# Kernel tuning notes

Hardware: AMD Instinct MI355X
Metric: run time of the kernel (lower is better)

## Reference

```python
import jax, jax.numpy as jnp
import numpy as np

C, C_H, N_HEAD = 256, 32, 8
LN_EPS = 1e-5


def setup_inputs() -> dict:
    key = jax.random.key(0)
    ks = jax.random.split(key, 10)
    B, S, I = 1, 256, 384
    hc = C_H * N_HEAD
    w = lambda k, shp: (jax.random.normal(k, shp, dtype=jnp.float32) * 0.02)
    return {
        "m": jax.random.normal(ks[0], (B, S, I, C), dtype=jnp.float32),
        "msa_mask": jnp.ones((B, S, I), dtype=jnp.float32),
        "gamma": jnp.ones((C,), dtype=jnp.float32),
        "beta": jnp.zeros((C,), dtype=jnp.float32),
        "Wq": w(ks[1], (C, hc)),
        "Wk": w(ks[2], (C, hc)),
        "Wv": w(ks[3], (C, hc)),
        "Wg": w(ks[4], (C, hc)),
        "bg": jnp.zeros((hc,), dtype=jnp.float32),
        "Wo": w(ks[5], (hc, C)),
        "bo": jnp.zeros((C,), dtype=jnp.float32),
    }


def reference(m, msa_mask, gamma, beta, Wq, Wk, Wv, Wg, bg, Wo, bo):
    B, S, I, _ = m.shape
    h, ch = N_HEAD, C_H
    # LayerNorm over channel dim
    mu = jnp.mean(m, axis=-1, keepdims=True)
    var = jnp.mean((m - mu) ** 2, axis=-1, keepdims=True)
    x = (m - mu) * jax.lax.rsqrt(var + LN_EPS) * gamma + beta  # (B,s,i,c)
    # projections -> (B,s,i,h,ch)
    q = (x @ Wq).reshape(B, S, I, h, ch)
    k = (x @ Wk).reshape(B, S, I, h, ch)
    v = (x @ Wv).reshape(B, S, I, h, ch)
    gate = jax.nn.sigmoid(x @ Wg + bg).reshape(B, S, I, h, ch)
    # column-wise attention over s, per column i and head h
    a = jnp.einsum("bsihc,btihc->bihst", q, k) / np.float32(np.sqrt(ch))
    # additive mask bias: msa_mask (B,s,i) -> (B,i,s) -> (B,i,1,1,s)
    bias = (1e9 * (jnp.swapaxes(msa_mask, -1, -2) - 1.0))[:, :, None, None, :]
    a = jax.nn.softmax(a + bias, axis=-1)
    # weighted values -> (B,s,i,h,ch)
    o = jnp.einsum("bihst,btihc->bsihc", a, v)
    o = (gate * o).reshape(B, S, I, h * ch)
    return o @ Wo + bo
```

## Files before the change

### kernel.cpp

```cpp
#include <hip/hip_runtime.h>

typedef unsigned short ushort_t;
typedef __attribute__((ext_vector_type(4))) short short4v;
typedef __attribute__((ext_vector_type(8))) short short8;
typedef __attribute__((ext_vector_type(4))) float floatx4;

#define SEQ 256
#define NI 384
#define CDIM 256
#define NH 8
#define CH 32
#define HC 256
#define NROW (SEQ * NI)
#define QKVG_N 1024

__device__ __forceinline__ float b2f(ushort_t u) {
  union { unsigned int i; float f; } z;
  z.i = ((unsigned int)u) << 16;
  return z.f;
}
__device__ __forceinline__ ushort_t f2b(float f) {
  union { float f; unsigned int i; } z;
  z.f = f;
  unsigned int x = z.i;
  unsigned int r = (x + 0x7fffu + ((x >> 16) & 1u)) >> 16;
  return (ushort_t)r;
}
__device__ __forceinline__ float ldx(const void* p, size_t i, int f32) {
  if (f32) return ((const float*)p)[i];
  return b2f(((const ushort_t*)p)[i]);
}

__global__ void detect_kernel(const unsigned int* __restrict__ g, int* __restrict__ flag) {
  *flag = (g[0] == 0x3F800000u) ? 1 : 0;
}

__global__ __launch_bounds__(256) void ln_norm_kernel(
    const void* __restrict__ m, const void* __restrict__ gamma, const void* __restrict__ beta,
    const int* __restrict__ pflag, ushort_t* __restrict__ xln) {
  int f32 = *pflag;
  int wave = threadIdx.x >> 6, lane = threadIdx.x & 63;
  int row = blockIdx.x * 4 + wave;
  size_t base = (size_t)row * CDIM + lane * 4;
  float v[4];
  float s1 = 0.f, s2 = 0.f;
  #pragma unroll
  for (int j = 0; j < 4; ++j) {
    v[j] = ldx(m, base + j, f32);
    s1 += v[j]; s2 += v[j] * v[j];
  }
  #pragma unroll
  for (int off = 1; off < 64; off <<= 1) {
    s1 += __shfl_xor(s1, off);
    s2 += __shfl_xor(s2, off);
  }
  float mu = s1 * (1.0f / CDIM);
  float var = s2 * (1.0f / CDIM) - mu * mu;
  float rstd = rsqrtf(var + 1e-5f);
  short4v o;
  #pragma unroll
  for (int j = 0; j < 4; ++j) {
    float g = ldx(gamma, lane * 4 + j, f32);
    float b = ldx(beta, lane * 4 + j, f32);
    o[j] = (short)f2b((v[j] - mu) * rstd * g + b);
  }
  *(short4v*)(xln + base) = o;
}

__global__ void transpose5(const void* a0, const void* a1, const void* a2, const void* a3,
                           const void* a4, const int* __restrict__ pflag,
                           ushort_t* __restrict__ Wqkvg, ushort_t* __restrict__ WoT) {
  int f32 = *pflag;
  int z = blockIdx.z;
  const void* src = (z == 0) ? a0 : (z == 1) ? a1 : (z == 2) ? a2 : (z == 3) ? a3 : a4;
  int x = blockIdx.x * 16 + threadIdx.x;
  int y = blockIdx.y * 16 + threadIdx.y;
  ushort_t val = f2b(ldx(src, (size_t)y * 256 + x, f32));
  if (z < 4) Wqkvg[((size_t)z * 256 + x) * 256 + y] = val;
  else       WoT[(size_t)x * 256 + y] = val;
}

#define LDT 56

__global__ __launch_bounds__(256) void gemm128(
    const ushort_t* __restrict__ A, const ushort_t* __restrict__ Bt,
    void* __restrict__ C, const void* __restrict__ bias, const int* __restrict__ pflag,
    int N, int epi, int CW, int i0, int mapA, int mapC) {
  int flag = *pflag;
  __shared__ __align__(16) ushort_t lA[128 * LDT];
  __shared__ __align__(16) ushort_t lB[128 * LDT];
  int tid = threadIdx.x;
  int m0 = blockIdx.x * 128, n0 = blockIdx.y * 128;
  int wave = tid >> 6, lane = tid & 63, lr = lane & 15, lq = lane >> 4;
  int wr = wave >> 1, wc = wave & 1;

  floatx4 acc[4][4];
  #pragma unroll
  for (int a = 0; a < 4; ++a)
    #pragma unroll
    for (int b = 0; b < 4; ++b) {
      acc[a][b][0] = 0.f; acc[a][b][1] = 0.f; acc[a][b][2] = 0.f; acc[a][b][3] = 0.f;
    }

  int row = tid >> 1, koff = (tid & 1) * 16;
  int rloc = m0 + row;
  int growA = mapA ? ((rloc / CW) * NI + i0 + (rloc % CW)) : rloc;
  const ushort_t* Ap = A + (size_t)growA * CDIM + koff;
  const ushort_t* Bp = Bt + (size_t)(n0 + row) * CDIM + koff;

  for (int k0 = 0; k0 < CDIM; k0 += 32) {
    short8 a0 = *(const short8*)(Ap + k0);
    short8 a1 = *(const short8*)(Ap + k0 + 8);
    short8 b0 = *(const short8*)(Bp + k0);
    short8 b1 = *(const short8*)(Bp + k0 + 8);
    *(short8*)&lA[row * LDT + koff] = a0;
    *(short8*)&lA[row * LDT + koff + 8] = a1;
    *(short8*)&lB[row * LDT + koff] = b0;
    *(short8*)&lB[row * LDT + koff + 8] = b1;
    __syncthreads();
    short8 af[4], bf[4];
    #pragma unroll
    for (int jm = 0; jm < 4; ++jm)
      af[jm] = *(const short8*)&lA[(wr * 64 + jm * 16 + lr) * LDT + lq * 8];
    #pragma unroll
    for (int jn = 0; jn < 4; ++jn)
      bf[jn] = *(const short8*)&lB[(wc * 64 + jn * 16 + lr) * LDT + lq * 8];
    #pragma unroll
    for (int jm = 0; jm < 4; ++jm)
      #pragma unroll
      for (int jn = 0; jn < 4; ++jn)
        acc[jm][jn] = __builtin_amdgcn_mfma_f32_16x16x32_bf16(af[jm], bf[jn], acc[jm][jn], 0, 0, 0);
    __syncthreads();
  }

  #pragma unroll
  for (int jm = 0; jm < 4; ++jm) {
    #pragma unroll
    for (int jn = 0; jn < 4; ++jn) {
      int col = n0 + wc * 64 + jn * 16 + lr;
      #pragma unroll
      for (int r = 0; r < 4; ++r) {
        int rl = m0 + wr * 64 + jm * 16 + lq * 4 + r;
        float val = acc[jm][jn][r];
        if (epi == 1) {
          if (col >= 768) {
            val += ldx(bias, col - 768, flag);
            val = 1.0f / (1.0f + __expf(-val));
          }
          ((ushort_t*)C)[(size_t)rl * N + col] = f2b(val);
        } else {
          val += ldx(bias, col, flag);
          int g = mapC ? ((rl / CW) * NI + i0 + (rl % CW)) : rl;
          if (flag) ((float*)C)[(size_t)g * N + col] = val;
          else      ((ushort_t*)C)[(size_t)g * N + col] = f2b(val);
        }
      }
    }
  }
}

#define KSTR 56
#define VSTR 264
#define PSTR 264

__global__ __launch_bounds__(256) void attn_mfma(
    const ushort_t* __restrict__ qkvg, const void* __restrict__ mask,
    const int* __restrict__ pflag, ushort_t* __restrict__ xln, int CW, int i0) {
  int f32 = *pflag;
  int il = blockIdx.x, h = blockIdx.y, qt = blockIdx.z;
  __shared__ __align__(16) ushort_t Kl[SEQ * KSTR];
  __shared__ __align__(16) ushort_t Vt[CH * VSTR];
  __shared__ __align__(16) ushort_t Pl[4 * 16 * PSTR];
  __shared__ float biasS[SEQ];
  int tid = threadIdx.x;

  {
    int t = tid;
    size_t base = ((size_t)t * CW + il) * QKVG_N + h * CH;
    short8 kv[4], vv[4];
    #pragma unroll
    for (int c4 = 0; c4 < 4; ++c4) {
      kv[c4] = *(const short8*)(qkvg + base + 256 + c4 * 8);
      vv[c4] = *(const short8*)(qkvg + base + 512 + c4 * 8);
    }
    #pragma unroll
    for (int c4 = 0; c4 < 4; ++c4) *(short8*)&Kl[t * KSTR + c4 * 8] = kv[c4];
    #pragma unroll
    for (int c4 = 0; c4 < 4; ++c4)
      #pragma unroll
      for (int j = 0; j < 8; ++j)
        Vt[(c4 * 8 + j) * VSTR + t] = (ushort_t)vv[c4][j];
    biasS[t] = 1e9f * (ldx(mask, (size_t)t * NI + i0 + il, f32) - 1.0f);
  }
  __syncthreads();

  int wave = tid >> 6, lane = tid & 63, lr = lane & 15, quad = lane >> 4;
  int sbase = qt * 64 + wave * 16;
  short8 qf = *(const short8*)(qkvg + ((size_t)(sbase + lr) * CW + il) * QKVG_N + h * CH + quad * 8);

  const float scale = 0.17677669529663687f;
  floatx4 s[16];
  #pragma unroll
  for (int tt = 0; tt < 16; ++tt) {
    short8 kb = *(const short8*)&Kl[(tt * 16 + lr) * KSTR + quad * 8];
    floatx4 z;
    z[0] = 0.f; z[1] = 0.f; z[2] = 0.f; z[3] = 0.f;
    s[tt] = __builtin_amdgcn_mfma_f32_16x16x32_bf16(qf, kb, z, 0, 0, 0);
  }
  #pragma unroll
  for (int tt = 0; tt < 16; ++tt) {
    float bv = biasS[tt * 16 + lr];
    #pragma unroll
    for (int r = 0; r < 4; ++r) s[tt][r] = s[tt][r] * scale + bv;
  }

  float mr[4], ls[4];
  #pragma unroll
  for (int r = 0; r < 4; ++r) {
    mr[r] = s[0][r];
    #pragma unroll
    for (int tt = 1; tt < 16; ++tt) mr[r] = fmaxf(mr[r], s[tt][r]);
  }
  #pragma unroll
  for (int msk = 1; msk < 16; msk <<= 1)
    #pragma unroll
    for (int r = 0; r < 4; ++r) mr[r] = fmaxf(mr[r], __shfl_xor(mr[r], msk));
  #pragma unroll
  for (int tt = 0; tt < 16; ++tt)
    #pragma unroll
    for (int r = 0; r < 4; ++r) s[tt][r] = __expf(s[tt][r] - mr[r]);
  #pragma unroll
  for (int r = 0; r < 4; ++r) {
    ls[r] = 0.f;
    #pragma unroll
    for (int tt = 0; tt < 16; ++tt) ls[r] += s[tt][r];
  }
  #pragma unroll
  for (int msk = 1; msk < 16; msk <<= 1)
    #pragma unroll
    for (int r = 0; r < 4; ++r) ls[r] += __shfl_xor(ls[r], msk);

  int pbase = wave * 16 * PSTR;
  #pragma unroll
  for (int tt = 0; tt < 16; ++tt)
    #pragma unroll
    for (int r = 0; r < 4; ++r)
      Pl[pbase + (quad * 4 + r) * PSTR + tt * 16 + lr] = f2b(s[tt][r]);

  floatx4 o0, o1;
  o0[0] = 0.f; o0[1] = 0.f; o0[2] = 0.f; o0[3] = 0.f;
  o1 = o0;
  #pragma unroll
  for (int tc = 0; tc < 8; ++tc) {
    short8 af = *(const short8*)&Pl[pbase + lr * PSTR + tc * 32 + quad * 8];
    short8 v0 = *(const short8*)&Vt[(0 + lr) * VSTR + tc * 32 + quad * 8];
    short8 v1 = *(const short8*)&Vt[(16 + lr) * VSTR + tc * 32 + quad * 8];
    o0 = __builtin_amdgcn_mfma_f32_16x16x32_bf16(af, v0, o0, 0, 0, 0);
    o1 = __builtin_amdgcn_mfma_f32_16x16x32_bf16(af, v1, o1, 0, 0, 0);
  }

  #pragma unroll
  for (int r = 0; r < 4; ++r) {
    int srow = sbase + quad * 4 + r;
    size_t grow = (size_t)srow * NI + i0 + il;
    size_t gbase = ((size_t)srow * CW + il) * QKVG_N + 768 + h * CH;
    float inv = 1.0f / ls[r];
    float g0 = b2f(qkvg[gbase + lr]);
    float g1 = b2f(qkvg[gbase + 16 + lr]);
    xln[grow * HC + h * CH + lr] = f2b(o0[r] * inv * g0);
    xln[grow * HC + h * CH + 16 + lr] = f2b(o1[r] * inv * g1);
  }
}

extern "C" void kernel_launch(void* const* d_in, const int* in_sizes, int n_in,
                              void* d_out, int out_size, void* d_ws, size_t ws_size,
                              hipStream_t stream) {
  const void* m     = d_in[0];
  const void* mask  = d_in[1];
  const void* gamma = d_in[2];
  const void* beta  = d_in[3];
  const void* Wq    = d_in[4];
  const void* Wk    = d_in[5];
  const void* Wv    = d_in[6];
  const void* Wg    = d_in[7];
  const void* bg    = d_in[8];
  const void* Wo    = d_in[9];
  const void* bo    = d_in[10];

  auto need = [](int nc) -> size_t {
    return 4096 + (size_t)QKVG_N * 256 * 2 + 256 * 256 * 2 + (size_t)NROW * CDIM * 2 +
           (size_t)SEQ * (NI / nc) * QKVG_N * 2 + 4096;
  };
  int nch = 1;
  while (nch < 8 && need(nch) > ws_size) nch *= 2;
  int CW = NI / nch;

  char* ws = (char*)d_ws;
  size_t off = 0;
  auto alloc = [&](size_t bytes) -> void* {
    void* p = ws + off;
    off += (bytes + 255) & ~(size_t)255;
    return p;
  };
  int* pflag       = (int*)alloc(256);
  ushort_t* WqkvgT = (ushort_t*)alloc((size_t)QKVG_N * 256 * 2);
  ushort_t* WoT    = (ushort_t*)alloc(256 * 256 * 2);
  ushort_t* xln    = (ushort_t*)alloc((size_t)NROW * CDIM * 2);
  ushort_t* qkvg   = (ushort_t*)alloc((size_t)SEQ * CW * QKVG_N * 2);

  detect_kernel<<<1, 1, 0, stream>>>((const unsigned int*)gamma, pflag);
  ln_norm_kernel<<<NROW / 4, 256, 0, stream>>>(m, gamma, beta, pflag, xln);
  transpose5<<<dim3(16, 16, 5), dim3(16, 16), 0, stream>>>(Wq, Wk, Wv, Wg, Wo, pflag,
                                                           WqkvgT, WoT);
  for (int c = 0; c < nch; ++c) {
    int i0 = c * CW;
    int M = SEQ * CW;
    gemm128<<<dim3(M / 128, QKVG_N / 128), 256, 0, stream>>>(
        xln, WqkvgT, qkvg, bg, pflag, QKVG_N, 1, CW, i0, 1, 0);
    attn_mfma<<<dim3(CW, NH, SEQ / 64), 256, 0, stream>>>(qkvg, mask, pflag, xln, CW, i0);
    gemm128<<<dim3(M / 128, CDIM / 128), 256, 0, stream>>>(
        xln, WoT, d_out, bo, pflag, CDIM, 2, CW, i0, 1, 1);
  }
}
```

Before: 582.5 us.

## Process all query tiles per attention block and vectorize layernorm loads

The attention kernel now has each block handle all 256 query rows for one column and head: each wave loops over four 16-row query tiles. K, V and the mask bias are therefore staged into shared memory once per (column, head) instead of four times. The grid shrinks by a factor of four, which reduces parallelism and could hurt occupancy or load balance. The layernorm kernel also switches to vector loads for m, gamma and beta, and the P-tile shared-memory stride changes from 264 to 260.

```diff
diff --git a/kernel.cpp b/kernel.cpp
--- a/kernel.cpp
+++ b/kernel.cpp
@@ -42,13 +42,25 @@
   int wave = threadIdx.x >> 6, lane = threadIdx.x & 63;
   int row = blockIdx.x * 4 + wave;
   size_t base = (size_t)row * CDIM + lane * 4;
-  float v[4];
+  float v[4], g[4], b[4];
+  if (f32) {
+    floatx4 vv = *(const floatx4*)((const float*)m + base);
+    floatx4 gg = *(const floatx4*)((const float*)gamma + lane * 4);
+    floatx4 bb = *(const floatx4*)((const float*)beta + lane * 4);
+    #pragma unroll
+    for (int j = 0; j < 4; ++j) { v[j] = vv[j]; g[j] = gg[j]; b[j] = bb[j]; }
+  } else {
+    short4v vv = *(const short4v*)((const ushort_t*)m + base);
+    short4v gg = *(const short4v*)((const ushort_t*)gamma + lane * 4);
+    short4v bb = *(const short4v*)((const ushort_t*)beta + lane * 4);
+    #pragma unroll
+    for (int j = 0; j < 4; ++j) {
+      v[j] = b2f((ushort_t)vv[j]); g[j] = b2f((ushort_t)gg[j]); b[j] = b2f((ushort_t)bb[j]);
+    }
+  }
   float s1 = 0.f, s2 = 0.f;
   #pragma unroll
-  for (int j = 0; j < 4; ++j) {
-    v[j] = ldx(m, base + j, f32);
-    s1 += v[j]; s2 += v[j] * v[j];
-  }
+  for (int j = 0; j < 4; ++j) { s1 += v[j]; s2 += v[j] * v[j]; }
   #pragma unroll
   for (int off = 1; off < 64; off <<= 1) {
     s1 += __shfl_xor(s1, off);
@@ -59,11 +71,7 @@
   float rstd = rsqrtf(var + 1e-5f);
   short4v o;
   #pragma unroll
-  for (int j = 0; j < 4; ++j) {
-    float g = ldx(gamma, lane * 4 + j, f32);
-    float b = ldx(beta, lane * 4 + j, f32);
-    o[j] = (short)f2b((v[j] - mu) * rstd * g + b);
-  }
+  for (int j = 0; j < 4; ++j) o[j] = (short)f2b((v[j] - mu) * rstd * g[j] + b[j]);
   *(short4v*)(xln + base) = o;
 }
 
@@ -161,13 +169,13 @@
 
 #define KSTR 56
 #define VSTR 264
-#define PSTR 264
+#define PSTR 260
 
 __global__ __launch_bounds__(256) void attn_mfma(
     const ushort_t* __restrict__ qkvg, const void* __restrict__ mask,
     const int* __restrict__ pflag, ushort_t* __restrict__ xln, int CW, int i0) {
   int f32 = *pflag;
-  int il = blockIdx.x, h = blockIdx.y, qt = blockIdx.z;
+  int il = blockIdx.x, h = blockIdx.y;
   __shared__ __align__(16) ushort_t Kl[SEQ * KSTR];
   __shared__ __align__(16) ushort_t Vt[CH * VSTR];
   __shared__ __align__(16) ushort_t Pl[4 * 16 * PSTR];
@@ -195,80 +203,88 @@
   __syncthreads();
 
   int wave = tid >> 6, lane = tid & 63, lr = lane & 15, quad = lane >> 4;
-  int sbase = qt * 64 + wave * 16;
-  short8 qf = *(const short8*)(qkvg + ((size_t)(sbase + lr) * CW + il) * QKVG_N + h * CH + quad * 8);
-
+  int pbase = wave * 16 * PSTR;
   const float scale = 0.17677669529663687f;
-  floatx4 s[16];
-  #pragma unroll
-  for (int tt = 0; tt < 16; ++tt) {
-    short8 kb = *(const short8*)&Kl[(tt * 16 + lr) * KSTR + quad * 8];
-    floatx4 z;
-    z[0] = 0.f; z[1] = 0.f; z[2] = 0.f; z[3] = 0.f;
-    s[tt] = __builtin_amdgcn_mfma_f32_16x16x32_bf16(qf, kb, z, 0, 0, 0);
-  }
-  #pragma unroll
-  for (int tt = 0; tt < 16; ++tt) {
-    float bv = biasS[tt * 16 + lr];
-    #pragma unroll
-    for (int r = 0; r < 4; ++r) s[tt][r] = s[tt][r] * scale + bv;
-  }
-
-  float mr[4], ls[4];
-  #pragma unroll
-  for (int r = 0; r < 4; ++r) {
-    mr[r] = s[0][r];
-    #pragma unroll
-    for (int tt = 1; tt < 16; ++tt) mr[r] = fmaxf(mr[r], s[tt][r]);
-  }
-  #pragma unroll
-  for (int msk = 1; msk < 16; msk <<= 1)
-    #pragma unroll
-    for (int r = 0; r < 4; ++r) mr[r] = fmaxf(mr[r], __shfl_xor(mr[r], msk));
-  #pragma unroll
-  for (int tt = 0; tt < 16; ++tt)
-    #pragma unroll
-    for (int r = 0; r < 4; ++r) s[tt][r] = __expf(s[tt][r] - mr[r]);
-  #pragma unroll
-  for (int r = 0; r < 4; ++r) {
-    ls[r] = 0.f;
-    #pragma unroll
-    for (int tt = 0; tt < 16; ++tt) ls[r] += s[tt][r];
-  }
-  #pragma unroll
-  for (int msk = 1; msk < 16; msk <<= 1)
-    #pragma unroll
-    for (int r = 0; r < 4; ++r) ls[r] += __shfl_xor(ls[r], msk);
-
-  int pbase = wave * 16 * PSTR;
-  #pragma unroll
-  for (int tt = 0; tt < 16; ++tt)
-    #pragma unroll
-    for (int r = 0; r < 4; ++r)
-      Pl[pbase + (quad * 4 + r) * PSTR + tt * 16 + lr] = f2b(s[tt][r]);
-
-  floatx4 o0, o1;
-  o0[0] = 0.f; o0[1] = 0.f; o0[2] = 0.f; o0[3] = 0.f;
-  o1 = o0;
-  #pragma unroll
-  for (int tc = 0; tc < 8; ++tc) {
-    short8 af = *(const short8*)&Pl[pbase + lr * PSTR + tc * 32 + quad * 8];
-    short8 v0 = *(const short8*)&Vt[(0 + lr) * VSTR + tc * 32 + quad * 8];
-    short8 v1 = *(const short8*)&Vt[(16 + lr) * VSTR + tc * 32 + quad * 8];
-    o0 = __builtin_amdgcn_mfma_f32_16x16x32_bf16(af, v0, o0, 0, 0, 0);
-    o1 = __builtin_amdgcn_mfma_f32_16x16x32_bf16(af, v1, o1, 0, 0, 0);
-  }
-
-  #pragma unroll
-  for (int r = 0; r < 4; ++r) {
-    int srow = sbase + quad * 4 + r;
-    size_t grow = (size_t)srow * NI + i0 + il;
-    size_t gbase = ((size_t)srow * CW + il) * QKVG_N + 768 + h * CH;
-    float inv = 1.0f / ls[r];
-    float g0 = b2f(qkvg[gbase + lr]);
-    float g1 = b2f(qkvg[gbase + 16 + lr]);
-    xln[grow * HC + h * CH + lr] = f2b(o0[r] * inv * g0);
-    xln[grow * HC + h * CH + 16 + lr] = f2b(o1[r] * inv * g1);
+
+  float bv[16];
+  #pragma unroll
+  for (int tt = 0; tt < 16; ++tt) bv[tt] = biasS[tt * 16 + lr];
+  short8 qf[4];
+  #pragma unroll
+  for (int mt = 0; mt < 4; ++mt)
+    qf[mt] = *(const short8*)(qkvg +
+        ((size_t)(wave * 64 + mt * 16 + lr) * CW + il) * QKVG_N + h * CH + quad * 8);
+
+  for (int mt = 0; mt < 4; ++mt) {
+    int sbase = wave * 64 + mt * 16;
+    floatx4 s[16];
+    #pragma unroll
+    for (int tt = 0; tt < 16; ++tt) {
+      short8 kb = *(const short8*)&Kl[(tt * 16 + lr) * KSTR + quad * 8];
+      floatx4 z;
+      z[0] = 0.f; z[1] = 0.f; z[2] = 0.f; z[3] = 0.f;
+      s[tt] = __builtin_amdgcn_mfma_f32_16x16x32_bf16(qf[mt], kb, z, 0, 0, 0);
+    }
+    #pragma unroll
+    for (int tt = 0; tt < 16; ++tt)
+      #pragma unroll
+      for (int r = 0; r < 4; ++r) s[tt][r] = s[tt][r] * scale + bv[tt];
+
+    float mr[4], ls[4];
+    #pragma unroll
+    for (int r = 0; r < 4; ++r) {
+      mr[r] = s[0][r];
+      #pragma unroll
+      for (int tt = 1; tt < 16; ++tt) mr[r] = fmaxf(mr[r], s[tt][r]);
+    }
+    #pragma unroll
+    for (int msk = 1; msk < 16; msk <<= 1)
+      #pragma unroll
+      for (int r = 0; r < 4; ++r) mr[r] = fmaxf(mr[r], __shfl_xor(mr[r], msk));
+    #pragma unroll
+    for (int tt = 0; tt < 16; ++tt)
+      #pragma unroll
+      for (int r = 0; r < 4; ++r) s[tt][r] = __expf(s[tt][r] - mr[r]);
+    #pragma unroll
+    for (int r = 0; r < 4; ++r) {
+      ls[r] = 0.f;
+      #pragma unroll
+      for (int tt = 0; tt < 16; ++tt) ls[r] += s[tt][r];
+    }
+    #pragma unroll
+    for (int msk = 1; msk < 16; msk <<= 1)
+      #pragma unroll
+      for (int r = 0; r < 4; ++r) ls[r] += __shfl_xor(ls[r], msk);
+
+    #pragma unroll
+    for (int tt = 0; tt < 16; ++tt)
+      #pragma unroll
+      for (int r = 0; r < 4; ++r)
+        Pl[pbase + (quad * 4 + r) * PSTR + tt * 16 + lr] = f2b(s[tt][r]);
+
+    floatx4 o0, o1;
+    o0[0] = 0.f; o0[1] = 0.f; o0[2] = 0.f; o0[3] = 0.f;
+    o1 = o0;
+    #pragma unroll
+    for (int tc = 0; tc < 8; ++tc) {
+      short8 af = *(const short8*)&Pl[pbase + lr * PSTR + tc * 32 + quad * 8];
+      short8 v0 = *(const short8*)&Vt[(0 + lr) * VSTR + tc * 32 + quad * 8];
+      short8 v1 = *(const short8*)&Vt[(16 + lr) * VSTR + tc * 32 + quad * 8];
+      o0 = __builtin_amdgcn_mfma_f32_16x16x32_bf16(af, v0, o0, 0, 0, 0);
+      o1 = __builtin_amdgcn_mfma_f32_16x16x32_bf16(af, v1, o1, 0, 0, 0);
+    }
+
+    #pragma unroll
+    for (int r = 0; r < 4; ++r) {
+      int srow = sbase + quad * 4 + r;
+      size_t grow = (size_t)srow * NI + i0 + il;
+      size_t gbase = ((size_t)srow * CW + il) * QKVG_N + 768 + h * CH;
+      float inv = 1.0f / ls[r];
+      float g0 = b2f(qkvg[gbase + lr]);
+      float g1 = b2f(qkvg[gbase + 16 + lr]);
+      xln[grow * HC + h * CH + lr] = f2b(o0[r] * inv * g0);
+      xln[grow * HC + h * CH + 16 + lr] = f2b(o1[r] * inv * g1);
+    }
   }
 }
 
@@ -317,7 +333,7 @@
     int M = SEQ * CW;
     gemm128<<<dim3(M / 128, QKVG_N / 128), 256, 0, stream>>>(
         xln, WqkvgT, qkvg, bg, pflag, QKVG_N, 1, CW, i0, 1, 0);
-    attn_mfma<<<dim3(CW, NH, SEQ / 64), 256, 0, stream>>>(qkvg, mask, pflag, xln, CW, i0);
+    attn_mfma<<<dim3(CW, NH), 256, 0, stream>>>(qkvg, mask, pflag, xln, CW, i0);
     gemm128<<<dim3(M / 128, CDIM / 128), 256, 0, stream>>>(
         xln, WoT, d_out, bo, pflag, CDIM, 2, CW, i0, 1, 1);
   }
```

After: 624.6 us. 7.2% more time.
